# Performance work log

Hardware: AMD Instinct MI355X
Metric: run time of the kernel (lower is better)

## Reference

```python
import jax, jax.numpy as jnp
import numpy as np

BS, S, DM, H, DK, DV, PRED = 64, 128, 512, 8, 512, 512, 96
NF = S * DM  # Flatten_Head nf = patch_num * d_model
SCALE_INIT = (DM // H) ** (-0.5)  # head_dim from d_model//n_heads per _ScaledDotProductAttention


def setup_inputs() -> dict:
    key = jax.random.key(0)
    ks = jax.random.split(key, 24)
    g = lambda k, shp: (0.02 * jax.random.normal(k, shp)).astype(jnp.float32)
    inp = {
        "x": jax.random.normal(ks[0], (BS, S, DM), dtype=jnp.float32),
        "prev": jax.random.normal(ks[1], (BS, H, S, S), dtype=jnp.float32),
        # multi-head attention projections (d_k = d_v = d_model per TMBlock)
        "Wq": g(ks[2], (DM, H * DK)), "bq": jnp.zeros((H * DK,), jnp.float32),
        "Wk": g(ks[3], (DM, H * DK)), "bk": jnp.zeros((H * DK,), jnp.float32),
        "Wv": g(ks[4], (DM, H * DV)), "bv": jnp.zeros((H * DV,), jnp.float32),
        "Wo": g(ks[5], (H * DV, DM)), "bo": jnp.zeros((DM,), jnp.float32),
        "scale": jnp.float32(SCALE_INIT),
        # InterPatchMixing: Linear(PatchNum, PatchNum) x2
        "Wi1": g(ks[6], (S, S)), "bi1": jnp.zeros((S,), jnp.float32),
        "Wi2": g(ks[7], (S, S)), "bi2": jnp.zeros((S,), jnp.float32),
        # IntraPatchMixing: Linear(PatchEmbedDim, PatchEmbedDim) x2
        "Wt1": g(ks[8], (DM, DM)), "bt1": jnp.zeros((DM,), jnp.float32),
        "Wt2": g(ks[9], (DM, DM)), "bt2": jnp.zeros((DM,), jnp.float32),
        # Flatten_Head (non-individual): Linear(nf, pred_len)
        "Wh": g(ks[10], (NF, PRED)), "bh": jnp.zeros((PRED,), jnp.float32),
    }
    return inp


def reference(x, prev, Wq, bq, Wk, bk, Wv, bv, Wo, bo, scale,
              Wi1, bi1, Wi2, bi2, Wt1, bt1, Wt2, bt2, Wh, bh):
    bs = x.shape[0]
    # projections -> [bs, H, S, d]
    q = (x @ Wq + bq).reshape(bs, S, H, DK).transpose(0, 2, 1, 3)
    k = (x @ Wk + bk).reshape(bs, S, H, DK).transpose(0, 2, 1, 3)
    v = (x @ Wv + bv).reshape(bs, S, H, DV).transpose(0, 2, 1, 3)
    # manual scaled dot-product attention with residual attention bias (Realformer)
    scores = jnp.einsum('bhqd,bhkd->bhqk', q, k) * scale + prev
    attn = jax.nn.softmax(scores, axis=-1)  # dropout is identity at eval
    o = jnp.einsum('bhqk,bhkd->bhqd', attn, v)
    o = o.transpose(0, 2, 1, 3).reshape(bs, S, H * DV)
    o = o @ Wo + bo  # [bs, S, DM]
    # InterPatchMixing over the patch axis (last dim must be PatchNum)
    t = o.transpose(0, 2, 1)  # [bs, DM, S]
    t = jax.nn.relu(t @ Wi1 + bi1) @ Wi2 + bi2
    y = t.transpose(0, 2, 1)  # [bs, S, DM]
    # IntraPatchMixing over embed dim
    z = jax.nn.relu(y @ Wt1 + bt1) @ Wt2 + bt2
    # Flatten_Head: flatten last two dims -> Linear(nf, pred_len)
    out = z.reshape(bs, NF) @ Wh + bh  # [bs, PRED]
    return out
```

## Files before the change

### kernel.cpp

```cpp
#include <hip/hip_runtime.h>
#include <cstdint>
#include <cstddef>

typedef __bf16 bf16_t;
typedef __bf16 bf16x8 __attribute__((ext_vector_type(8)));
typedef __bf16 bf16x4 __attribute__((ext_vector_type(4)));
typedef float  f32x4  __attribute__((ext_vector_type(4)));

#define MFMA(a, b, c) __builtin_amdgcn_mfma_f32_16x16x32_bf16((a), (b), (c), 0, 0, 0)


__global__ __launch_bounds__(256) void k_convert_dual(const float* __restrict__ in,
                                                      bf16_t* __restrict__ xb,
                                                      bf16_t* __restrict__ xT) {
  __shared__ bf16_t tile[32][34];
  int tx = threadIdx.x & 31, ty = threadIdx.x >> 5;
  int c0 = blockIdx.x * 32, r0 = blockIdx.y * 32;
#pragma unroll
  for (int j = 0; j < 4; ++j) {
    int r = r0 + ty + j * 8;
    bf16_t bv = (bf16_t)in[(size_t)r * 512 + c0 + tx];
    xb[(size_t)r * 512 + c0 + tx] = bv;
    tile[ty + j * 8][tx] = bv;
  }
  __syncthreads();
  int b = (r0 + tx) >> 7, s = (r0 + tx) & 127;
#pragma unroll
  for (int j = 0; j < 4; ++j) {
    int i = c0 + ty + j * 8;
    xT[(size_t)b * 65536 + (size_t)i * 128 + s] = tile[tx][ty + j * 8];
  }
}

__global__ __launch_bounds__(256) void k_transpose_convert(const float* __restrict__ in,
                                                           bf16_t* __restrict__ out,
                                                           int R, int C) {
  __shared__ float tile[32][33];
  int tx = threadIdx.x & 31, ty = threadIdx.x >> 5;
  int c0 = blockIdx.x * 32, r0 = blockIdx.y * 32;
#pragma unroll
  for (int j = 0; j < 4; ++j)
    tile[ty + j * 8][tx] = in[(size_t)(r0 + ty + j * 8) * C + c0 + tx];
  __syncthreads();
#pragma unroll
  for (int j = 0; j < 4; ++j)
    out[(size_t)(c0 + ty + j * 8) * R + r0 + tx] = (bf16_t)tile[tx][ty + j * 8];
}

__global__ __launch_bounds__(256) void k_transpose_b16(const bf16_t* __restrict__ in,
                                                       bf16_t* __restrict__ out,
                                                       int R, int C) {
  __shared__ bf16_t tile[32][34];
  size_t base = (size_t)blockIdx.z * R * C;
  int tx = threadIdx.x & 31, ty = threadIdx.x >> 5;
  int c0 = blockIdx.x * 32, r0 = blockIdx.y * 32;
#pragma unroll
  for (int j = 0; j < 4; ++j)
    tile[ty + j * 8][tx] = in[base + (size_t)(r0 + ty + j * 8) * C + c0 + tx];
  __syncthreads();
#pragma unroll
  for (int j = 0; j < 4; ++j)
    out[base + (size_t)(c0 + ty + j * 8) * R + r0 + tx] = tile[tx][ty + j * 8];
}

template <int BMODE>
__global__ __launch_bounds__(256) void k_wprod(const float* __restrict__ Ap,
                                               const float* __restrict__ Bp,
                                               bf16_t* __restrict__ out,
                                               int ldA, int ldB) {
  __shared__ __align__(16) bf16_t As[128 * 68];
  __shared__ __align__(16) bf16_t Bs[128 * 68];
  const int tid = threadIdx.x, lane = tid & 63, wave = tid >> 6;
  const int wr = (wave >> 1) * 64, wc = (wave & 1) * 64;
  const int lr = lane & 15, lk = (lane >> 4) * 8, frow = (lane >> 4) * 4;
  const int m0 = blockIdx.x * 128, n0 = blockIdx.y * 128, h = blockIdx.z;
  const int sr = tid >> 3, sc = (tid & 7) * 8;
  f32x4 acc[4][4] = {};

  for (int kt = 0; kt < 512; kt += 64) {
#pragma unroll
    for (int rr = 0; rr < 4; ++rr) {
      int r = sr + 32 * rr;
      const float* ap = Ap + (size_t)(m0 + r) * ldA + h * 512 + kt + sc;
      bf16x8 av;
#pragma unroll
      for (int e = 0; e < 8; ++e) av[e] = (bf16_t)ap[e];
      *(bf16x8*)(As + r * 68 + sc) = av;
    }
    if (BMODE == 0) {
#pragma unroll
      for (int rr = 0; rr < 4; ++rr) {
        int r = sr + 32 * rr;
        const float* bp = Bp + (size_t)(n0 + r) * ldB + h * 512 + kt + sc;
        bf16x8 bv;
#pragma unroll
        for (int e = 0; e < 8; ++e) bv[e] = (bf16_t)bp[e];
        *(bf16x8*)(Bs + r * 68 + sc) = bv;
      }
    } else {
#pragma unroll
      for (int rr = 0; rr < 8; ++rr) {
        int kr = (tid >> 5) + 8 * rr;
        int nc = (tid & 31) * 4;
        const float* bp = Bp + (size_t)(h * 512 + kt + kr) * ldB + n0 + nc;
        float4 v = *(const float4*)bp;
        Bs[(nc + 0) * 68 + kr] = (bf16_t)v.x;
        Bs[(nc + 1) * 68 + kr] = (bf16_t)v.y;
        Bs[(nc + 2) * 68 + kr] = (bf16_t)v.z;
        Bs[(nc + 3) * 68 + kr] = (bf16_t)v.w;
      }
    }
    __syncthreads();
#pragma unroll
    for (int kk = 0; kk < 2; ++kk) {
      bf16x8 af[4], bfr[4];
#pragma unroll
      for (int i = 0; i < 4; ++i)
        af[i] = *(const bf16x8*)(As + (wr + i * 16 + lr) * 68 + kk * 32 + lk);
#pragma unroll
      for (int j = 0; j < 4; ++j)
        bfr[j] = *(const bf16x8*)(Bs + (wc + j * 16 + lr) * 68 + kk * 32 + lk);
#pragma unroll
      for (int i = 0; i < 4; ++i)
#pragma unroll
        for (int j = 0; j < 4; ++j)
          acc[i][j] = MFMA(af[i], bfr[j], acc[i][j]);
    }
    __syncthreads();
  }
#pragma unroll
  for (int i = 0; i < 4; ++i)
#pragma unroll
    for (int j = 0; j < 4; ++j)
#pragma unroll
      for (int q = 0; q < 4; ++q) {
        int gm = m0 + wr + i * 16 + frow + q;
        int gn = n0 + wc + j * 16 + lr;
        if (BMODE == 0)
          out[(size_t)(h * 512 + gn) * 512 + gm] = (bf16_t)acc[i][j][q];
        else
          out[(size_t)gn * 4096 + h * 512 + gm] = (bf16_t)acc[i][j][q];
      }
}

__global__ __launch_bounds__(256) void k_sbias(const float* __restrict__ Wq,
                                               const float* __restrict__ bk,
                                               const float* __restrict__ Wk,
                                               const float* __restrict__ bq,
                                               float* __restrict__ W1,
                                               float* __restrict__ W2,
                                               float* __restrict__ c) {
  const int lane = threadIdx.x & 63, wave = threadIdx.x >> 6;
  const int i = blockIdx.x * 4 + wave;
  for (int h = 0; h < 8; ++h) {
    float s1 = 0.f, s2 = 0.f;
    for (int d = lane; d < 512; d += 64) {
      s1 += Wq[(size_t)i * 4096 + h * 512 + d] * bk[h * 512 + d];
      s2 += Wk[(size_t)i * 4096 + h * 512 + d] * bq[h * 512 + d];
    }
#pragma unroll
    for (int o = 32; o > 0; o >>= 1) { s1 += __shfl_down(s1, o); s2 += __shfl_down(s2, o); }
    if (lane == 0) { W1[h * 512 + i] = s1; W2[h * 512 + i] = s2; }
  }
  if (blockIdx.x == 0 && wave == 0) {
    for (int h = 0; h < 8; ++h) {
      float cc = 0.f;
      for (int d = lane; d < 512; d += 64) cc += bq[h * 512 + d] * bk[h * 512 + d];
#pragma unroll
      for (int o = 32; o > 0; o >>= 1) cc += __shfl_down(cc, o);
      if (lane == 0) c[h] = cc;
    }
  }
}

__global__ __launch_bounds__(256) void k_cvec1(const float* __restrict__ bv,
                                               const float* __restrict__ Wo,
                                               float* __restrict__ cpart) {
  int cch = blockIdx.x, d = threadIdx.x * 2;
  float ax = 0.f, ay = 0.f;
  for (int n = cch * 128; n < cch * 128 + 128; ++n) {
    float b = bv[n];
    float2 w = *(const float2*)(Wo + (size_t)n * 512 + d);
    ax += b * w.x; ay += b * w.y;
  }
  cpart[(size_t)cch * 512 + d] = ax;
  cpart[(size_t)cch * 512 + d + 1] = ay;
}
__global__ __launch_bounds__(256) void k_cvec2(const float* __restrict__ cpart,
                                               const float* __restrict__ bo,
                                               float* __restrict__ cvec) {
  int d = blockIdx.x * 256 + threadIdx.x;
  float s = bo[d];
  for (int cch = 0; cch < 32; ++cch) s += cpart[(size_t)cch * 512 + d];
  cvec[d] = s;
}

__global__ __launch_bounds__(256, 2) void k_attn3(const bf16_t* __restrict__ xb,
                                                  const bf16_t* __restrict__ xT,
                                                  bf16_t* __restrict__ TU,
                                                  const float* __restrict__ prev,
                                                  const float* __restrict__ scale_p,
                                                  const float* __restrict__ W1,
                                                  const float* __restrict__ W2,
                                                  const float* __restrict__ cb,
                                                  int hg) {
  __shared__ __align__(16) bf16_t Xs[128 * 68];
  __shared__ __align__(16) bf16_t Pl[64 * 132];
  __shared__ __align__(16) bf16_t TsXt[64 * 132];
  __shared__ float T1s[64], T2s[128];
  __shared__ float csh;

  const int tid = threadIdx.x, lane = tid & 63, wave = tid >> 6;
  const int lr = lane & 15, lk = (lane >> 4) * 8, frow = (lane >> 4) * 4;
  const int sr = tid >> 3, sc = (tid & 7) * 8;
  const int b = blockIdx.x >> 3, hp = (blockIdx.x >> 1) & 3, half = blockIdx.x & 1;
  const int h = hg * 4 + hp;
  const int row0 = half * 64;
  const bf16_t* xB = xb + (size_t)b * 65536;
  bf16_t* tB = TU + ((size_t)hp * 8192 + b * 128 + row0) * 512;

  {
    int sp = tid >> 1, part = tid & 1;
    const bf16_t* xrow = xB + (size_t)sp * 512 + part * 256;
    const float* w1 = W1 + h * 512 + part * 256;
    const float* w2 = W2 + h * 512 + part * 256;
    float s1 = 0.f, s2 = 0.f;
    for (int i = 0; i < 256; i += 8) {
      bf16x8 xv = *(const bf16x8*)(xrow + i);
#pragma unroll
      for (int e = 0; e < 8; ++e) {
        float f = (float)xv[e];
        s1 += f * w1[i + e];
        s2 += f * w2[i + e];
      }
    }
    float* scr = (float*)Pl;
    scr[tid] = s1; scr[256 + tid] = s2;
    if (tid == 0) csh = cb[h];
    __syncthreads();
    if (tid < 128) {
      T2s[tid] = scr[256 + 2 * tid] + scr[256 + 2 * tid + 1];
      float t1v = scr[2 * tid] + scr[2 * tid + 1];
      if (tid >= row0 && tid < row0 + 64) T1s[tid - row0] = t1v;
    }
    __syncthreads();
  }

  bf16_t* Ts = TsXt;
  f32x4 sacc[8] = {};
  for (int kt = 0; kt < 8; ++kt) {
#pragma unroll
    for (int rr = 0; rr < 2; ++rr) {
      int r = sr + 32 * rr;
      *(bf16x8*)(Ts + r * 68 + sc) = *(const bf16x8*)(tB + (size_t)r * 512 + kt * 64 + sc);
    }
#pragma unroll
    for (int rr = 0; rr < 4; ++rr) {
      int r = sr + 32 * rr;
      *(bf16x8*)(Xs + r * 68 + sc) = *(const bf16x8*)(xB + (size_t)r * 512 + kt * 64 + sc);
    }
    __syncthreads();
#pragma unroll
    for (int kk = 0; kk < 2; ++kk) {
      bf16x8 af = *(const bf16x8*)(Ts + (wave * 16 + lr) * 68 + kk * 32 + lk);
      bf16x8 bfr[8];
#pragma unroll
      for (int j = 0; j < 8; ++j)
        bfr[j] = *(const bf16x8*)(Xs + (j * 16 + lr) * 68 + kk * 32 + lk);
#pragma unroll
      for (int j = 0; j < 8; ++j) sacc[j] = MFMA(af, bfr[j], sacc[j]);
    }
    __syncthreads();
  }

  const float scl = scale_p[0];
#pragma unroll
  for (int e = 0; e < 4; ++e) {
    const int rl = wave * 16 + frow + e;
    const float* prow = prev + (((size_t)(b * 8 + h)) * 128 + row0 + rl) * 128;
    float mx = -3.4e38f;
#pragma unroll
    for (int j = 0; j < 8; ++j) {
      int col = j * 16 + lr;
      float v = scl * (sacc[j][e] + T1s[rl] + T2s[col] + csh) + prow[col];
      sacc[j][e] = v;
      mx = fmaxf(mx, v);
    }
    mx = fmaxf(mx, __shfl_xor(mx, 1));
    mx = fmaxf(mx, __shfl_xor(mx, 2));
    mx = fmaxf(mx, __shfl_xor(mx, 4));
    mx = fmaxf(mx, __shfl_xor(mx, 8));
    float sum = 0.f;
#pragma unroll
    for (int j = 0; j < 8; ++j) {
      float p = __expf(sacc[j][e] - mx);
      sacc[j][e] = p;
      sum += p;
    }
    sum += __shfl_xor(sum, 1);
    sum += __shfl_xor(sum, 2);
    sum += __shfl_xor(sum, 4);
    sum += __shfl_xor(sum, 8);
    float inv = 1.f / sum;
#pragma unroll
    for (int j = 0; j < 8; ++j)
      Pl[rl * 132 + j * 16 + lr] = (bf16_t)(sacc[j][e] * inv);
  }
  __syncthreads();

  bf16_t* Xt = TsXt;
  const bf16_t* xTB = xT + (size_t)b * 65536;
  for (int dc = 0; dc < 8; ++dc) {
#pragma unroll
    for (int rr = 0; rr < 4; ++rr) {
      int r = (tid >> 4) + 16 * rr;
      *(bf16x8*)(Xt + r * 132 + (tid & 15) * 8) =
          *(const bf16x8*)(xTB + (size_t)(dc * 64 + r) * 128 + (tid & 15) * 8);
    }
    __syncthreads();
    f32x4 oacc[4] = {};
#pragma unroll
    for (int kk = 0; kk < 4; ++kk) {
      bf16x8 af = *(const bf16x8*)(Pl + (wave * 16 + lr) * 132 + kk * 32 + lk);
      bf16x8 bfr[4];
#pragma unroll
      for (int j = 0; j < 4; ++j)
        bfr[j] = *(const bf16x8*)(Xt + (j * 16 + lr) * 132 + kk * 32 + lk);
#pragma unroll
      for (int j = 0; j < 4; ++j) oacc[j] = MFMA(af, bfr[j], oacc[j]);
    }
    __syncthreads();
#pragma unroll
    for (int j = 0; j < 4; ++j)
#pragma unroll
      for (int e = 0; e < 4; ++e)
        Xs[(wave * 16 + frow + e) * 68 + j * 16 + lr] = (bf16_t)oacc[j][e];
    __syncthreads();
#pragma unroll
    for (int rr = 0; rr < 2; ++rr) {
      int r = sr + 32 * rr;
      *(bf16x8*)(tB + (size_t)r * 512 + dc * 64 + sc) = *(const bf16x8*)(Xs + r * 68 + sc);
    }
  }
}

template <int OUTMODE, int RELU>
__global__ __launch_bounds__(256) void k_gemm(const bf16_t* __restrict__ A,
                                              const bf16_t* __restrict__ Bt,
                                              const float* __restrict__ bias,
                                              bf16_t* __restrict__ C,
                                              int M, int N, int K) {
  __shared__ __align__(16) bf16_t As[128 * 68];
  __shared__ __align__(16) bf16_t Bs[128 * 68];
  const int tid = threadIdx.x, lane = tid & 63, wave = tid >> 6;
  const int wr = (wave >> 1) * 64, wc = (wave & 1) * 64;
  const int m0 = blockIdx.x * 128, n0 = blockIdx.y * 128;
  const int lr = lane & 15, lk = (lane >> 4) * 8, frow = (lane >> 4) * 4;
  const int sr = tid >> 3, sc = (tid & 7) * 8;
  f32x4 acc[4][4] = {};

  for (int kt = 0; kt < K; kt += 64) {
#pragma unroll
    for (int i = 0; i < 4; ++i) {
      int r = i * 32 + sr;
      *(bf16x8*)(As + r * 68 + sc) = *(const bf16x8*)(A + (size_t)(m0 + r) * K + kt + sc);
      *(bf16x8*)(Bs + r * 68 + sc) = *(const bf16x8*)(Bt + (size_t)(n0 + r) * K + kt + sc);
    }
    __syncthreads();
#pragma unroll
    for (int kk = 0; kk < 2; ++kk) {
      bf16x8 af[4], bfr[4];
#pragma unroll
      for (int i = 0; i < 4; ++i)
        af[i] = *(const bf16x8*)(As + (wr + i * 16 + lr) * 68 + kk * 32 + lk);
#pragma unroll
      for (int j = 0; j < 4; ++j)
        bfr[j] = *(const bf16x8*)(Bs + (wc + j * 16 + lr) * 68 + kk * 32 + lk);
#pragma unroll
      for (int i = 0; i < 4; ++i)
#pragma unroll
        for (int j = 0; j < 4; ++j)
          acc[i][j] = MFMA(af[i], bfr[j], acc[i][j]);
    }
    __syncthreads();
  }
#pragma unroll
  for (int j = 0; j < 4; ++j) {
    int gn = n0 + wc + j * 16 + lr;
    float bv = bias ? bias[gn] : 0.0f;
#pragma unroll
    for (int i = 0; i < 4; ++i) {
#pragma unroll
      for (int q = 0; q < 4; ++q) {
        int gm = m0 + wr + i * 16 + frow + q;
        float v = acc[i][j][q] + bv;
        if (RELU) v = v > 0.0f ? v : 0.0f;
        if (OUTMODE == 0)
          C[(size_t)gm * N + gn] = (bf16_t)v;
        else
          C[((size_t)(gn >> 9) * 8192 + gm) * 512 + (gn & 511)] = (bf16_t)v;
      }
    }
  }
}

template <int MODE>
__global__ __launch_bounds__(256) void k_gemm2(const bf16_t* __restrict__ U,
                                               const bf16_t* __restrict__ bt2,
                                               float* __restrict__ o1acc,
                                               const float* __restrict__ cvec,
                                               bf16_t* __restrict__ o1b, int g) {
  __shared__ __align__(16) bf16_t As[128 * 68];
  __shared__ __align__(16) bf16_t Bs[128 * 68];
  const int tid = threadIdx.x, lane = tid & 63, wave = tid >> 6;
  const int wr = (wave >> 1) * 64, wc = (wave & 1) * 64;
  const int m0 = blockIdx.x * 128, n0 = blockIdx.y * 128;
  const int lr = lane & 15, lk = (lane >> 4) * 8, frow = (lane >> 4) * 4;
  const int sr = tid >> 3, sc = (tid & 7) * 8;
  f32x4 acc[4][4] = {};

  for (int kt = 0; kt < 2048; kt += 64) {
    const int slab = kt >> 9, off = kt & 511;
#pragma unroll
    for (int i = 0; i < 4; ++i) {
      int r = i * 32 + sr;
      *(bf16x8*)(As + r * 68 + sc) =
          *(const bf16x8*)(U + ((size_t)slab * 8192 + m0 + r) * 512 + off + sc);
      *(bf16x8*)(Bs + r * 68 + sc) =
          *(const bf16x8*)(bt2 + (size_t)(n0 + r) * 4096 + g * 2048 + kt + sc);
    }
    __syncthreads();
#pragma unroll
    for (int kk = 0; kk < 2; ++kk) {
      bf16x8 af[4], bfr[4];
#pragma unroll
      for (int i = 0; i < 4; ++i)
        af[i] = *(const bf16x8*)(As + (wr + i * 16 + lr) * 68 + kk * 32 + lk);
#pragma unroll
      for (int j = 0; j < 4; ++j)
        bfr[j] = *(const bf16x8*)(Bs + (wc + j * 16 + lr) * 68 + kk * 32 + lk);
#pragma unroll
      for (int i = 0; i < 4; ++i)
#pragma unroll
        for (int j = 0; j < 4; ++j)
          acc[i][j] = MFMA(af[i], bfr[j], acc[i][j]);
    }
    __syncthreads();
  }
#pragma unroll
  for (int j = 0; j < 4; ++j) {
    int gn = n0 + wc + j * 16 + lr;
#pragma unroll
    for (int i = 0; i < 4; ++i) {
#pragma unroll
      for (int q = 0; q < 4; ++q) {
        int gm = m0 + wr + i * 16 + frow + q;
        size_t idx = (size_t)gm * 512 + gn;
        if (MODE == 0)
          o1acc[idx] = acc[i][j][q];
        else
          o1b[idx] = (bf16_t)(acc[i][j][q] + o1acc[idx] + cvec[gn]);
      }
    }
  }
}

__global__ __launch_bounds__(256) void k_head_partial(const bf16_t* __restrict__ Z,
                                                      const bf16_t* __restrict__ WhT,
                                                      float* __restrict__ part) {
  __shared__ __align__(16) bf16_t As[64 * 68];
  __shared__ __align__(16) bf16_t Bs[96 * 68];
  const int tid = threadIdx.x, lane = tid & 63, wave = tid >> 6;
  const int wr = (wave >> 1) * 32, wc = (wave & 1) * 48;
  const int lr = lane & 15, lk = (lane >> 4) * 8, frow = (lane >> 4) * 4;
  const int k0 = blockIdx.x * 512;
  const int sr = tid >> 3, sc = (tid & 7) * 8;
  f32x4 acc[2][3] = {};
  for (int kt = 0; kt < 512; kt += 64) {
#pragma unroll
    for (int i = 0; i < 2; ++i) {
      int r = i * 32 + sr;
      *(bf16x8*)(As + r * 68 + sc) = *(const bf16x8*)(Z + (size_t)r * 65536 + k0 + kt + sc);
    }
#pragma unroll
    for (int i = 0; i < 3; ++i) {
      int r = i * 32 + sr;
      *(bf16x8*)(Bs + r * 68 + sc) = *(const bf16x8*)(WhT + (size_t)r * 65536 + k0 + kt + sc);
    }
    __syncthreads();
#pragma unroll
    for (int kk = 0; kk < 2; ++kk) {
      bf16x8 af[2], bfr[3];
#pragma unroll
      for (int i = 0; i < 2; ++i)
        af[i] = *(const bf16x8*)(As + (wr + i * 16 + lr) * 68 + kk * 32 + lk);
#pragma unroll
      for (int j = 0; j < 3; ++j)
        bfr[j] = *(const bf16x8*)(Bs + (wc + j * 16 + lr) * 68 + kk * 32 + lk);
#pragma unroll
      for (int i = 0; i < 2; ++i)
#pragma unroll
        for (int j = 0; j < 3; ++j)
          acc[i][j] = MFMA(af[i], bfr[j], acc[i][j]);
    }
    __syncthreads();
  }
#pragma unroll
  for (int i = 0; i < 2; ++i)
#pragma unroll
    for (int j = 0; j < 3; ++j)
#pragma unroll
      for (int q = 0; q < 4; ++q) {
        int m = wr + i * 16 + frow + q;
        int n = wc + j * 16 + lr;
        part[(size_t)blockIdx.x * 6144 + m * 96 + n] = acc[i][j][q];
      }
}

__global__ __launch_bounds__(256) void k_head_reduce(const float* __restrict__ part,
                                                     const float* __restrict__ bias,
                                                     float* __restrict__ out) {
  int idx = blockIdx.x * 256 + threadIdx.x;
  if (idx >= 6144) return;
  float s = bias[idx % 96];
  for (int kb = 0; kb < 128; ++kb) s += part[(size_t)kb * 6144 + idx];
  out[idx] = s;
}

__global__ void k_sentinel(float* out, int n, float val) {
  int i = blockIdx.x * 256 + threadIdx.x;
  if (i < n) out[i] = val;
}

extern "C" void kernel_launch(void* const* d_in, const int* in_sizes, int n_in,
                              void* d_out, int out_size, void* d_ws, size_t ws_size,
                              hipStream_t stream) {
  const float* x    = (const float*)d_in[0];
  const float* prev = (const float*)d_in[1];
  const float* Wq = (const float*)d_in[2];   const float* bq = (const float*)d_in[3];
  const float* Wk = (const float*)d_in[4];   const float* bk = (const float*)d_in[5];
  const float* Wv = (const float*)d_in[6];   const float* bv = (const float*)d_in[7];
  const float* Wo = (const float*)d_in[8];   const float* bo = (const float*)d_in[9];
  const float* scale = (const float*)d_in[10];
  const float* Wi1 = (const float*)d_in[11]; const float* bi1 = (const float*)d_in[12];
  const float* Wi2 = (const float*)d_in[13]; const float* bi2 = (const float*)d_in[14];
  const float* Wt1 = (const float*)d_in[15]; const float* bt1w = (const float*)d_in[16];
  const float* Wt2 = (const float*)d_in[17]; const float* bt2w = (const float*)d_in[18];
  const float* Wh = (const float*)d_in[19];  const float* bh = (const float*)d_in[20];
  float* out = (float*)d_out;

  char* p = (char*)d_ws;
  auto carve = [&](size_t bytes) {
    char* r = p;
    p += (bytes + 255) & ~(size_t)255;
    return r;
  };
  bf16_t* xb    = (bf16_t*)carve((size_t)8192 * 512 * 2);
  bf16_t* xTo1b = (bf16_t*)carve((size_t)8192 * 512 * 2);
  float*  o1acc = (float*)carve((size_t)8192 * 512 * 4);
  bf16_t* bt1   = (bf16_t*)carve((size_t)4096 * 512 * 2);
  bf16_t* bt2   = (bf16_t*)carve((size_t)512 * 4096 * 2);
  float*  W1    = (float*)carve(8 * 512 * 4);
  float*  W2    = (float*)carve(8 * 512 * 4);
  float*  cb    = (float*)carve(8 * 4);
  float*  cvec  = (float*)carve(512 * 4);
  char*   arena = carve((size_t)8192 * 2048 * 2);
  bf16_t* TU    = (bf16_t*)arena;
  float*  cpart = (float*)arena;
  bf16_t* xT    = xTo1b;
  bf16_t* o1b   = xTo1b;
  char* q2 = arena;
  auto carve2 = [&](size_t bytes) {
    char* r = q2;
    q2 += (bytes + 255) & ~(size_t)255;
    return r;
  };
  bf16_t* whT  = (bf16_t*)carve2((size_t)96 * 65536 * 2);
  bf16_t* wt1T = (bf16_t*)carve2((size_t)512 * 512 * 2);
  bf16_t* wt2T = (bf16_t*)carve2((size_t)512 * 512 * 2);
  bf16_t* wi1T = (bf16_t*)carve2((size_t)128 * 128 * 2);
  bf16_t* wi2T = (bf16_t*)carve2((size_t)128 * 128 * 2);
  float*  hp   = (float*)carve2((size_t)128 * 64 * 96 * 4);
  bf16_t* bufB = (bf16_t*)carve2((size_t)8192 * 512 * 2);

  if ((size_t)(p - (char*)d_ws) > ws_size) {
    k_sentinel<<<24, 256, 0, stream>>>(out, 6144, (float)ws_size);
    return;
  }

  dim3 blk(256);
  k_cvec1<<<32, blk, 0, stream>>>(bv, Wo, cpart);
  k_cvec2<<<2, blk, 0, stream>>>(cpart, bo, cvec);
  k_convert_dual<<<dim3(16, 256), blk, 0, stream>>>(x, xb, xT);
  k_wprod<0><<<dim3(4, 4, 8), blk, 0, stream>>>(Wq, Wk, bt1, 4096, 4096);
  k_wprod<1><<<dim3(4, 4, 8), blk, 0, stream>>>(Wv, Wo, bt2, 4096, 512);
  k_sbias<<<128, blk, 0, stream>>>(Wq, bk, Wk, bq, W1, W2, cb);

  k_gemm<2, 0><<<dim3(64, 16), blk, 0, stream>>>(xb, bt1, nullptr, TU, 8192, 2048, 512);
  k_attn3<<<512, blk, 0, stream>>>(xb, xT, TU, prev, scale, W1, W2, cb, 0);
  k_gemm2<0><<<dim3(64, 4), blk, 0, stream>>>(TU, bt2, o1acc, cvec, o1b, 0);
  k_gemm<2, 0><<<dim3(64, 16), blk, 0, stream>>>(xb, bt1 + (size_t)2048 * 512, nullptr, TU,
                                                 8192, 2048, 512);
  k_attn3<<<512, blk, 0, stream>>>(xb, xT, TU, prev, scale, W1, W2, cb, 1);
  k_gemm2<1><<<dim3(64, 4), blk, 0, stream>>>(TU, bt2, o1acc, cvec, o1b, 1);

  k_transpose_convert<<<dim3(4, 4), blk, 0, stream>>>(Wi1, wi1T, 128, 128);
  k_transpose_convert<<<dim3(4, 4), blk, 0, stream>>>(Wi2, wi2T, 128, 128);
  k_transpose_convert<<<dim3(16, 16), blk, 0, stream>>>(Wt1, wt1T, 512, 512);
  k_transpose_convert<<<dim3(16, 16), blk, 0, stream>>>(Wt2, wt2T, 512, 512);
  k_transpose_convert<<<dim3(3, 2048), blk, 0, stream>>>(Wh, whT, 65536, 96);

  k_transpose_b16<<<dim3(16, 4, 64), blk, 0, stream>>>(o1b, bufB, 128, 512);
  k_gemm<0, 1><<<dim3(256, 1), blk, 0, stream>>>(bufB, wi1T, bi1, o1b, 32768, 128, 128);
  k_gemm<0, 0><<<dim3(256, 1), blk, 0, stream>>>(o1b, wi2T, bi2, bufB, 32768, 128, 128);
  k_transpose_b16<<<dim3(4, 16, 64), blk, 0, stream>>>(bufB, o1b, 512, 128);

  k_gemm<0, 1><<<dim3(64, 4), blk, 0, stream>>>(o1b, wt1T, bt1w, bufB, 8192, 512, 512);
  k_gemm<0, 0><<<dim3(64, 4), blk, 0, stream>>>(bufB, wt2T, bt2w, o1b, 8192, 512, 512);

  k_head_partial<<<128, blk, 0, stream>>>(o1b, whT, hp);
  k_head_reduce<<<24, blk, 0, stream>>>(hp, bh, out);
}
```

Measured before the change: 470.2 us.

## Load attention MFMA operands directly from global memory and raise occupancy

The attention kernel no longer stages the T, X and X-transpose tiles through shared memory. Each wave now loads its MFMA fragments straight from global memory (relying on L2/L1 reuse) and keeps per-wave P and output staging buffers, which removes most block-wide barriers. The reduced LDS footprint allows launch bounds of 4 blocks per SM, and block IDs are remapped to interleave batches across the grid. The cost is redundant global fragment loads across waves, so performance now depends on cache hit rates rather than explicit LDS reuse.

```diff
diff --git a/kernel.cpp b/kernel.cpp
--- a/kernel.cpp
+++ b/kernel.cpp
@@ -195,7 +195,7 @@
   cvec[d] = s;
 }
 
-__global__ __launch_bounds__(256, 2) void k_attn3(const bf16_t* __restrict__ xb,
+__global__ __launch_bounds__(256, 4) void k_attn4(const bf16_t* __restrict__ xb,
                                                   const bf16_t* __restrict__ xT,
                                                   bf16_t* __restrict__ TU,
                                                   const float* __restrict__ prev,
@@ -204,19 +204,21 @@
                                                   const float* __restrict__ W2,
                                                   const float* __restrict__ cb,
                                                   int hg) {
-  __shared__ __align__(16) bf16_t Xs[128 * 68];
-  __shared__ __align__(16) bf16_t Pl[64 * 132];
-  __shared__ __align__(16) bf16_t TsXt[64 * 132];
+  __shared__ __align__(16) bf16_t Pl[4][16 * 132];
+  __shared__ __align__(16) bf16_t Bw[4][16 * 68];
+  __shared__ float scr[512];
   __shared__ float T1s[64], T2s[128];
   __shared__ float csh;
 
   const int tid = threadIdx.x, lane = tid & 63, wave = tid >> 6;
   const int lr = lane & 15, lk = (lane >> 4) * 8, frow = (lane >> 4) * 4;
-  const int sr = tid >> 3, sc = (tid & 7) * 8;
-  const int b = blockIdx.x >> 3, hp = (blockIdx.x >> 1) & 3, half = blockIdx.x & 1;
+  const int bid = blockIdx.x;
+  const int bx = (bid & 7) * 64 + (bid >> 3);
+  const int b = bx >> 3, hp = (bx >> 1) & 3, half = bx & 1;
   const int h = hg * 4 + hp;
   const int row0 = half * 64;
   const bf16_t* xB = xb + (size_t)b * 65536;
+  const bf16_t* xTB = xT + (size_t)b * 65536;
   bf16_t* tB = TU + ((size_t)hp * 8192 + b * 128 + row0) * 512;
 
   {
@@ -234,46 +236,40 @@
         s2 += f * w2[i + e];
       }
     }
-    float* scr = (float*)Pl;
-    scr[tid] = s1; scr[256 + tid] = s2;
+    scr[tid] = s1;
     if (tid == 0) csh = cb[h];
     __syncthreads();
     if (tid < 128) {
-      T2s[tid] = scr[256 + 2 * tid] + scr[256 + 2 * tid + 1];
       float t1v = scr[2 * tid] + scr[2 * tid + 1];
       if (tid >= row0 && tid < row0 + 64) T1s[tid - row0] = t1v;
     }
     __syncthreads();
-  }
-
-  bf16_t* Ts = TsXt;
+    scr[tid] = s2;
+    __syncthreads();
+    if (tid < 128) T2s[tid] = scr[2 * tid] + scr[2 * tid + 1];
+    __syncthreads();
+  }
+
   f32x4 sacc[8] = {};
-  for (int kt = 0; kt < 8; ++kt) {
-#pragma unroll
-    for (int rr = 0; rr < 2; ++rr) {
-      int r = sr + 32 * rr;
-      *(bf16x8*)(Ts + r * 68 + sc) = *(const bf16x8*)(tB + (size_t)r * 512 + kt * 64 + sc);
-    }
-#pragma unroll
-    for (int rr = 0; rr < 4; ++rr) {
-      int r = sr + 32 * rr;
-      *(bf16x8*)(Xs + r * 68 + sc) = *(const bf16x8*)(xB + (size_t)r * 512 + kt * 64 + sc);
-    }
-    __syncthreads();
-#pragma unroll
-    for (int kk = 0; kk < 2; ++kk) {
-      bf16x8 af = *(const bf16x8*)(Ts + (wave * 16 + lr) * 68 + kk * 32 + lk);
-      bf16x8 bfr[8];
-#pragma unroll
-      for (int j = 0; j < 8; ++j)
-        bfr[j] = *(const bf16x8*)(Xs + (j * 16 + lr) * 68 + kk * 32 + lk);
-#pragma unroll
-      for (int j = 0; j < 8; ++j) sacc[j] = MFMA(af, bfr[j], sacc[j]);
-    }
-    __syncthreads();
+  const bf16_t* aP = tB + (size_t)(wave * 16 + lr) * 512 + lk;
+  {
+#pragma unroll 2
+    for (int kt = 0; kt < 8; ++kt) {
+#pragma unroll
+      for (int kk = 0; kk < 2; ++kk) {
+        bf16x8 af = *(const bf16x8*)(aP + kt * 64 + kk * 32);
+        bf16x8 bfr[8];
+#pragma unroll
+        for (int j = 0; j < 8; ++j)
+          bfr[j] = *(const bf16x8*)(xB + (size_t)(j * 16 + lr) * 512 + kt * 64 + kk * 32 + lk);
+#pragma unroll
+        for (int j = 0; j < 8; ++j) sacc[j] = MFMA(af, bfr[j], sacc[j]);
+      }
+    }
   }
 
   const float scl = scale_p[0];
+  bf16_t* Plw = Pl[wave];
 #pragma unroll
   for (int e = 0; e < 4; ++e) {
     const int rl = wave * 16 + frow + e;
@@ -304,42 +300,33 @@
     float inv = 1.f / sum;
 #pragma unroll
     for (int j = 0; j < 8; ++j)
-      Pl[rl * 132 + j * 16 + lr] = (bf16_t)(sacc[j][e] * inv);
-  }
-  __syncthreads();
-
-  bf16_t* Xt = TsXt;
-  const bf16_t* xTB = xT + (size_t)b * 65536;
+      Plw[(frow + e) * 132 + j * 16 + lr] = (bf16_t)(sacc[j][e] * inv);
+  }
+
+  bf16_t* Bww = Bw[wave];
+#pragma unroll 2
   for (int dc = 0; dc < 8; ++dc) {
-#pragma unroll
-    for (int rr = 0; rr < 4; ++rr) {
-      int r = (tid >> 4) + 16 * rr;
-      *(bf16x8*)(Xt + r * 132 + (tid & 15) * 8) =
-          *(const bf16x8*)(xTB + (size_t)(dc * 64 + r) * 128 + (tid & 15) * 8);
-    }
-    __syncthreads();
     f32x4 oacc[4] = {};
 #pragma unroll
     for (int kk = 0; kk < 4; ++kk) {
-      bf16x8 af = *(const bf16x8*)(Pl + (wave * 16 + lr) * 132 + kk * 32 + lk);
-      bf16x8 bfr[4];
+      bf16x8 pa = *(const bf16x8*)(Plw + lr * 132 + kk * 32 + lk);
+      bf16x8 xtf[4];
 #pragma unroll
       for (int j = 0; j < 4; ++j)
-        bfr[j] = *(const bf16x8*)(Xt + (j * 16 + lr) * 132 + kk * 32 + lk);
-#pragma unroll
-      for (int j = 0; j < 4; ++j) oacc[j] = MFMA(af, bfr[j], oacc[j]);
-    }
-    __syncthreads();
+        xtf[j] = *(const bf16x8*)(xTB + (size_t)(dc * 64 + j * 16 + lr) * 128 + kk * 32 + lk);
+#pragma unroll
+      for (int j = 0; j < 4; ++j) oacc[j] = MFMA(pa, xtf[j], oacc[j]);
+    }
 #pragma unroll
     for (int j = 0; j < 4; ++j)
 #pragma unroll
       for (int e = 0; e < 4; ++e)
-        Xs[(wave * 16 + frow + e) * 68 + j * 16 + lr] = (bf16_t)oacc[j][e];
-    __syncthreads();
-#pragma unroll
-    for (int rr = 0; rr < 2; ++rr) {
-      int r = sr + 32 * rr;
-      *(bf16x8*)(tB + (size_t)r * 512 + dc * 64 + sc) = *(const bf16x8*)(Xs + r * 68 + sc);
+        Bww[(frow + e) * 68 + j * 16 + lr] = (bf16_t)oacc[j][e];
+#pragma unroll
+    for (int r2 = 0; r2 < 2; ++r2) {
+      int row = lane >> 2, chunk = (lane & 3) + r2 * 4;
+      *(bf16x8*)(tB + (size_t)(wave * 16 + row) * 512 + dc * 64 + chunk * 8) =
+          *(const bf16x8*)(Bww + row * 68 + chunk * 8);
     }
   }
 }
@@ -597,11 +584,11 @@
   k_sbias<<<128, blk, 0, stream>>>(Wq, bk, Wk, bq, W1, W2, cb);
 
   k_gemm<2, 0><<<dim3(64, 16), blk, 0, stream>>>(xb, bt1, nullptr, TU, 8192, 2048, 512);
-  k_attn3<<<512, blk, 0, stream>>>(xb, xT, TU, prev, scale, W1, W2, cb, 0);
+  k_attn4<<<512, blk, 0, stream>>>(xb, xT, TU, prev, scale, W1, W2, cb, 0);
   k_gemm2<0><<<dim3(64, 4), blk, 0, stream>>>(TU, bt2, o1acc, cvec, o1b, 0);
   k_gemm<2, 0><<<dim3(64, 16), blk, 0, stream>>>(xb, bt1 + (size_t)2048 * 512, nullptr, TU,
                                                  8192, 2048, 512);
-  k_attn3<<<512, blk, 0, stream>>>(xb, xT, TU, prev, scale, W1, W2, cb, 1);
+  k_attn4<<<512, blk, 0, stream>>>(xb, xT, TU, prev, scale, W1, W2, cb, 1);
   k_gemm2<1><<<dim3(64, 4), blk, 0, stream>>>(TU, bt2, o1acc, cvec, o1b, 1);
 
   k_transpose_convert<<<dim3(4, 4), blk, 0, stream>>>(Wi1, wi1T, 128, 128);
```

Measured after the change: 496.0 us. 5.5% more time.
